# Performance work log

Measured on AMD Instinct MI355X. Metric: run time of the kernel, lower is better.

The kernel has to match this reference:

```python
import jax, jax.numpy as jnp
import numpy as np

B, T, F_, H1, H2, HEADS = 64, 128, 64, 32, 64, 4
E = H2 * F_  # embed_dim = hidden_dims[-1] * feats = 4096


def conv2d(x, w, b):
    # x: [b,c,H,W], w: [o,c,kh,kw], SAME padding (kernel 3 -> pad 1)
    y = jax.lax.conv_general_dilated(x, w, (1, 1), 'SAME',
                                     dimension_numbers=('NCHW', 'OIHW', 'NCHW'))
    return y + b[None, :, None, None]


def gru_layer(xs, h0, wg, bg, wc, bc):
    # xs: [b,t,c,H,W]; h0: [b,h,H,W]. Standard ConvGRU cell:
    #   r,u = sigmoid(conv([x,h])); cand = tanh(conv([x, r*h]))
    #   h' = (1-u)*h + u*cand
    def step(h, x):
        g = conv2d(jnp.concatenate([x, h], axis=1), wg, bg)
        r, u = jnp.split(jax.nn.sigmoid(g), 2, axis=1)
        cand = jnp.tanh(conv2d(jnp.concatenate([x, r * h], axis=1), wc, bc))
        h_next = (1.0 - u) * h + u * cand
        return h_next, h_next
    hT, ys = jax.lax.scan(step, h0, jnp.swapaxes(xs, 0, 1))
    return jnp.swapaxes(ys, 0, 1), hT  # [b,t,h,H,W], [b,h,H,W]


def mha(q, k, v, w_qkv, b_qkv, w_out, b_out):
    # q: [b,1,E], k/v: [b,t,E]; torch nn.MultiheadAttention (eval, no dropout)
    wq, wk, wv = jnp.split(w_qkv, 3, axis=0)
    bq, bk, bv = jnp.split(b_qkv, 3, axis=0)
    dh = E // HEADS
    def heads(x, w, bb):
        y = x @ w.T + bb
        b_, l_, _ = y.shape
        return y.reshape(b_, l_, HEADS, dh).transpose(0, 2, 1, 3)  # [b,h,l,dh]
    qh, kh, vh = heads(q, wq, bq), heads(k, wk, bk), heads(v, wv, bv)
    scores = jnp.einsum('bhqd,bhkd->bhqk', qh, kh) / jnp.sqrt(jnp.float32(dh))
    attn = jax.nn.softmax(scores, axis=-1)
    ctx = jnp.einsum('bhqk,bhkd->bhqd', attn, vh)
    ctx = ctx.transpose(0, 2, 1, 3).reshape(q.shape[0], q.shape[1], E)
    return ctx @ w_out.T + b_out


def setup_inputs() -> dict:
    key = jax.random.key(0)
    ks = jax.random.split(key, 24)
    s = 0.05
    d = {'x': jax.random.normal(ks[0], (B, T, F_), dtype=jnp.float32)}
    # encoder layer 0: in=1, h=H1; layer 1: in=H1, h=H2
    d['wg_e0'] = jax.random.normal(ks[1], (2 * H1, 1 + H1, 3, 3)) * s
    d['bg_e0'] = jnp.zeros((2 * H1,))
    d['wc_e0'] = jax.random.normal(ks[2], (H1, 1 + H1, 3, 3)) * s
    d['bc_e0'] = jnp.zeros((H1,))
    d['wg_e1'] = jax.random.normal(ks[3], (2 * H2, H1 + H2, 3, 3)) * s
    d['bg_e1'] = jnp.zeros((2 * H2,))
    d['wc_e1'] = jax.random.normal(ks[4], (H2, H1 + H2, 3, 3)) * s
    d['bc_e1'] = jnp.zeros((H2,))
    # decoder: input dim = 2*H2; hidden dims reversed [H2, H1]
    d['wg_d0'] = jax.random.normal(ks[5], (2 * H2, 2 * H2 + H2, 3, 3)) * s
    d['bg_d0'] = jnp.zeros((2 * H2,))
    d['wc_d0'] = jax.random.normal(ks[6], (H2, 2 * H2 + H2, 3, 3)) * s
    d['bc_d0'] = jnp.zeros((H2,))
    d['wg_d1'] = jax.random.normal(ks[7], (2 * H1, H2 + H1, 3, 3)) * s
    d['bg_d1'] = jnp.zeros((2 * H1,))
    d['wc_d1'] = jax.random.normal(ks[8], (H1, H2 + H1, 3, 3)) * s
    d['bc_d1'] = jnp.zeros((H1,))
    d['w_qkv'] = jax.random.normal(ks[9], (3 * E, E)) * (1.0 / np.sqrt(E))
    d['b_qkv'] = jnp.zeros((3 * E,))
    d['w_out'] = jax.random.normal(ks[10], (E, E)) * (1.0 / np.sqrt(E))
    d['b_out'] = jnp.zeros((E,))
    d['w_fin'] = jax.random.normal(ks[11], (1, H1, 1, 1)) * s
    d['b_fin'] = jnp.zeros((1,))
    return d


def reference(x, wg_e0, bg_e0, wc_e0, bc_e0, wg_e1, bg_e1, wc_e1, bc_e1,
              wg_d0, bg_d0, wc_d0, bc_d0, wg_d1, bg_d1, wc_d1, bc_d1,
              w_qkv, b_qkv, w_out, b_out, w_fin, b_fin):
    b, t, f = x.shape
    xr = x.reshape(b, t, 1, f, 1)
    # encoder (2 ConvGRU layers, zero init states)
    y0, h0 = gru_layer(xr, jnp.zeros((b, H1, f, 1), x.dtype), wg_e0, bg_e0, wc_e0, bc_e0)
    y1, h1 = gru_layer(y0, jnp.zeros((b, H2, f, 1), x.dtype), wg_e1, bg_e1, wc_e1, bc_e1)
    # attention bottleneck: query = last hidden, memory = encoder outputs
    query = h1.reshape(b, 1, E)
    memory = y1.reshape(b, t, E)
    context = mha(query, memory, memory, w_qkv, b_qkv, w_out, b_out)  # [b,1,E]
    ctx = context.reshape(b, 1, H2, f, 1)
    dec_in = jnp.concatenate([y1, jnp.broadcast_to(ctx, (b, t, H2, f, 1))], axis=2)
    # decoder init states: encoder last states reversed -> [h1 (H2), h0 (H1)]
    z0, _ = gru_layer(dec_in, h1, wg_d0, bg_d0, wc_d0, bc_d0)
    z1, _ = gru_layer(z0, h0, wg_d1, bg_d1, wc_d1, bc_d1)  # [b,t,H1,f,1]
    # final 1x1 conv applied per timestep == channel contraction
    rec = jnp.einsum('btcfw,oc->btofw', z1, w_fin[:, :, 0, 0]) + b_fin[None, None, :, None, None]
    return rec.reshape(b, t, f)
```

## Files before the change

kernel.cpp:

```cpp
#include <hip/hip_runtime.h>
#include <cstdint>


#define B_  64
#define T_  128
#define TC  32
#define NCH 4

__device__ __forceinline__ float wsum(float v) {
#pragma unroll
  for (int m = 32; m > 0; m >>= 1) v += __shfl_xor(v, m, 64);
  return v;
}
__device__ __forceinline__ float wmaxr(float v) {
#pragma unroll
  for (int m = 32; m > 0; m >>= 1) v = fmaxf(v, __shfl_xor(v, m, 64));
  return v;
}
__device__ __forceinline__ float sigmoidf_(float x) {
  return 1.f / (1.f + __expf(-x));
}
__device__ __forceinline__ float tanhf_(float x) {
  x = fminf(fmaxf(x, -15.f), 15.f);
  float e2 = __expf(2.f * x);
  return (e2 - 1.f) / (e2 + 1.f);
}

struct PackArgs {
  const float* src[16];
  float* dst[16];
  int intot[16];
  int ic0[16];
  int icn[16];
  int oc[16];
};

__global__ __launch_bounds__(256) void pack_all_kernel(PackArgs pa) {
  const int j = blockIdx.y;
  const int icN = pa.icn[j];
  const int total = pa.oc[j] * icN * 3;
  const int i = blockIdx.x * 256 + threadIdx.x;
  if (i >= total) return;
  const int per_oc = icN * 3;
  const int oc = i / per_oc;
  const int rem = i - oc * per_oc;
  const int ic = rem / 3, dk = rem - ic * 3;
  pa.dst[j][i] =
      pa.src[j][((size_t)(oc * pa.intot[j] + pa.ic0[j] + ic) * 3 + dk) * 3 + 1];
}

template <int INC, int OG, int OCC>
__device__ __forceinline__ void conv_x_body(
    float (*sin_)[72], int tid, int btl,
    const float* __restrict__ seq, int seqC, size_t sB,
    const float* __restrict__ ctx,
    const float* __restrict__ Wgx, const float* __restrict__ Wcx,
    const float* __restrict__ bg, const float* __restrict__ bc,
    float* __restrict__ out) {
  constexpr int OCT = OG + OCC;
  constexpr int NJ = OG / 32;
  constexpr int NJC = OCC / 32;
  const int b = btl >> 5;
  const int tl = btl & 31;
  const int ocg = tid >> 3;
  const int f0 = (tid & 7) << 3;

  for (int idx = tid; idx < INC * 72; idx += 256) {
    int ic = idx / 72, ff = idx - ic * 72;
    float v = 0.f;
    if (ff >= 1 && ff <= 64) {
      int fs = ff - 1;
      v = (ic < seqC)
              ? seq[(size_t)b * sB + (size_t)tl * seqC * 64 + ic * 64 + fs]
              : ctx[((size_t)b * (INC - seqC) + (ic - seqC)) * 64 + fs];
    }
    sin_[ic][ff] = v;
  }
  __syncthreads();

  if constexpr (INC >= 4) {
    {
      float acc[NJ][8];
#pragma unroll
      for (int j = 0; j < NJ; ++j) {
        float bb = bg[ocg + 32 * j];
#pragma unroll
        for (int ff = 0; ff < 8; ++ff) acc[j][ff] = bb;
      }
      for (int ic0 = 0; ic0 < INC; ic0 += 4) {
        float hv[4][10];
#pragma unroll
        for (int q = 0; q < 4; ++q) {
          float4 a4 = *(const float4*)&sin_[ic0 + q][f0];
          float4 b4 = *(const float4*)&sin_[ic0 + q][f0 + 4];
          float2 c2 = *(const float2*)&sin_[ic0 + q][f0 + 8];
          hv[q][0] = a4.x; hv[q][1] = a4.y; hv[q][2] = a4.z; hv[q][3] = a4.w;
          hv[q][4] = b4.x; hv[q][5] = b4.y; hv[q][6] = b4.z; hv[q][7] = b4.w;
          hv[q][8] = c2.x; hv[q][9] = c2.y;
        }
#pragma unroll
        for (int j = 0; j < NJ; ++j) {
          const int oc = ocg + 32 * j;
          const float4* w4 = (const float4*)(Wgx + ((size_t)oc * INC + ic0) * 3);
          float4 wa = w4[0], wb = w4[1], wc4 = w4[2];
          const float wt[12] = {wa.x, wa.y, wa.z, wa.w, wb.x, wb.y, wb.z, wb.w,
                                wc4.x, wc4.y, wc4.z, wc4.w};
#pragma unroll
          for (int q = 0; q < 4; ++q) {
            const float w0 = wt[3 * q], w1 = wt[3 * q + 1], w2 = wt[3 * q + 2];
#pragma unroll
            for (int ff = 0; ff < 8; ++ff)
              acc[j][ff] = fmaf(w0, hv[q][ff], fmaf(w1, hv[q][ff + 1], fmaf(w2, hv[q][ff + 2], acc[j][ff])));
          }
        }
      }
#pragma unroll
      for (int j = 0; j < NJ; ++j) {
        float* dst = out + ((size_t)btl * OCT + ocg + 32 * j) * 64 + f0;
        *(float4*)dst = make_float4(acc[j][0], acc[j][1], acc[j][2], acc[j][3]);
        *(float4*)(dst + 4) = make_float4(acc[j][4], acc[j][5], acc[j][6], acc[j][7]);
      }
    }
    {
      float acc[NJC][8];
#pragma unroll
      for (int j = 0; j < NJC; ++j) {
        float bb = bc[ocg + 32 * j];
#pragma unroll
        for (int ff = 0; ff < 8; ++ff) acc[j][ff] = bb;
      }
      for (int ic0 = 0; ic0 < INC; ic0 += 4) {
        float hv[4][10];
#pragma unroll
        for (int q = 0; q < 4; ++q) {
          float4 a4 = *(const float4*)&sin_[ic0 + q][f0];
          float4 b4 = *(const float4*)&sin_[ic0 + q][f0 + 4];
          float2 c2 = *(const float2*)&sin_[ic0 + q][f0 + 8];
          hv[q][0] = a4.x; hv[q][1] = a4.y; hv[q][2] = a4.z; hv[q][3] = a4.w;
          hv[q][4] = b4.x; hv[q][5] = b4.y; hv[q][6] = b4.z; hv[q][7] = b4.w;
          hv[q][8] = c2.x; hv[q][9] = c2.y;
        }
#pragma unroll
        for (int j = 0; j < NJC; ++j) {
          const int oc = ocg + 32 * j;
          const float4* w4 = (const float4*)(Wcx + ((size_t)oc * INC + ic0) * 3);
          float4 wa = w4[0], wb = w4[1], wc4 = w4[2];
          const float wt[12] = {wa.x, wa.y, wa.z, wa.w, wb.x, wb.y, wb.z, wb.w,
                                wc4.x, wc4.y, wc4.z, wc4.w};
#pragma unroll
          for (int q = 0; q < 4; ++q) {
            const float w0 = wt[3 * q], w1 = wt[3 * q + 1], w2 = wt[3 * q + 2];
#pragma unroll
            for (int ff = 0; ff < 8; ++ff)
              acc[j][ff] = fmaf(w0, hv[q][ff], fmaf(w1, hv[q][ff + 1], fmaf(w2, hv[q][ff + 2], acc[j][ff])));
          }
        }
      }
#pragma unroll
      for (int j = 0; j < NJC; ++j) {
        float* dst = out + ((size_t)btl * OCT + OG + ocg + 32 * j) * 64 + f0;
        *(float4*)dst = make_float4(acc[j][0], acc[j][1], acc[j][2], acc[j][3]);
        *(float4*)(dst + 4) = make_float4(acc[j][4], acc[j][5], acc[j][6], acc[j][7]);
      }
    }
  } else {
    float hv[10];
    {
      float4 a4 = *(const float4*)&sin_[0][f0];
      float4 b4 = *(const float4*)&sin_[0][f0 + 4];
      float2 c2 = *(const float2*)&sin_[0][f0 + 8];
      hv[0] = a4.x; hv[1] = a4.y; hv[2] = a4.z; hv[3] = a4.w;
      hv[4] = b4.x; hv[5] = b4.y; hv[6] = b4.z; hv[7] = b4.w;
      hv[8] = c2.x; hv[9] = c2.y;
    }
#pragma unroll
    for (int j = 0; j < NJ; ++j) {
      const int oc = ocg + 32 * j;
      const float w0 = Wgx[oc * 3], w1 = Wgx[oc * 3 + 1], w2 = Wgx[oc * 3 + 2];
      float acc[8];
#pragma unroll
      for (int ff = 0; ff < 8; ++ff)
        acc[ff] = fmaf(w0, hv[ff], fmaf(w1, hv[ff + 1], fmaf(w2, hv[ff + 2], bg[oc])));
      float* dst = out + ((size_t)btl * OCT + oc) * 64 + f0;
      *(float4*)dst = make_float4(acc[0], acc[1], acc[2], acc[3]);
      *(float4*)(dst + 4) = make_float4(acc[4], acc[5], acc[6], acc[7]);
    }
#pragma unroll
    for (int j = 0; j < NJC; ++j) {
      const int oc = ocg + 32 * j;
      const float w0 = Wcx[oc * 3], w1 = Wcx[oc * 3 + 1], w2 = Wcx[oc * 3 + 2];
      float acc[8];
#pragma unroll
      for (int ff = 0; ff < 8; ++ff)
        acc[ff] = fmaf(w0, hv[ff], fmaf(w1, hv[ff + 1], fmaf(w2, hv[ff + 2], bc[oc])));
      float* dst = out + ((size_t)btl * OCT + OG + oc) * 64 + f0;
      *(float4*)dst = make_float4(acc[0], acc[1], acc[2], acc[3]);
      *(float4*)(dst + 4) = make_float4(acc[4], acc[5], acc[6], acc[7]);
    }
  }
}

template <int INC, int OG, int OCC>
__global__ __launch_bounds__(256) void conv_x_kernel(
    const float* __restrict__ seq, int seqC, size_t sB,
    const float* __restrict__ ctx,
    const float* __restrict__ Wgx, const float* __restrict__ Wcx,
    const float* __restrict__ bg, const float* __restrict__ bc,
    float* __restrict__ out) {
  __shared__ float sin_[INC][72];
  conv_x_body<INC, OG, OCC>(sin_, threadIdx.x, blockIdx.x, seq, seqC, sB, ctx,
                            Wgx, Wcx, bg, bc, out);
}

__device__ __forceinline__ void final_body(
    int tid, int tile, const float* __restrict__ z1c,
    const float* __restrict__ wfin, const float* __restrict__ bfin,
    float* __restrict__ out, int tOff) {
  const int idx = tile * 256 + tid;
  const int f = idx & 63;
  const int tl = (idx >> 6) & 31;
  const int b = idx >> 11;
  const float* zp = z1c + ((size_t)b * TC + tl) * 2048 + f;
  float a = bfin[0];
#pragma unroll
  for (int c = 0; c < 32; ++c) a = fmaf(wfin[c], zp[c * 64], a);
  out[(size_t)b * 8192 + (size_t)(tOff + tl) * 64 + f] = a;
}

__global__ __launch_bounds__(256) void final_kernel(
    const float* __restrict__ z1c,
    const float* __restrict__ wfin, const float* __restrict__ bfin,
    float* __restrict__ out, int tOff) {
  final_body(threadIdx.x, blockIdx.x, z1c, wfin, bfin, out, tOff);
}

template <int HC>
__device__ __forceinline__ void gru_body(
    float* smem,
    const float* __restrict__ A, const float* __restrict__ Wgh,
    const float* __restrict__ Wch, const float* hinit,
    float* __restrict__ Y, size_t yB, float* hfinal, int b) {
  constexpr int NR = HC / 32;
  constexpr int OG = 2 * HC;
  constexpr int OCT = 3 * HC;
  float(*Hs)[68] = (float(*)[68])smem;
  float(*Rs)[68] = (float(*)[68])(smem + HC * 68);
  const int tid = threadIdx.x;
  const int ocg = tid >> 4;
  const int f0 = (tid & 15) << 2;
  const int im = (f0 == 0) ? 0 : f0 - 1;
  const bool lo = (f0 == 0), hi = (f0 == 60);

  float hreg[NR][4];
#pragma unroll
  for (int r = 0; r < NR; ++r) {
    const int oc = ocg + 32 * r;
    const float4 v = *(const float4*)(hinit + ((size_t)b * HC + oc) * 64 + f0);
    hreg[r][0] = v.x; hreg[r][1] = v.y; hreg[r][2] = v.z; hreg[r][3] = v.w;
    *(float4*)&Hs[oc][f0] = v;
  }
  __syncthreads();

  for (int tl = 0; tl < TC; ++tl) {
    const float* Abt = A + ((size_t)b * TC + tl) * (OCT * 64);
    float accr[NR][4], accu[NR][4], accc[NR][4];
#pragma unroll
    for (int r = 0; r < NR; ++r) {
      const int oc = ocg + 32 * r;
      const float4 vr = *(const float4*)(Abt + (size_t)oc * 64 + f0);
      const float4 vu = *(const float4*)(Abt + (size_t)(HC + oc) * 64 + f0);
      const float4 vc = *(const float4*)(Abt + (size_t)(OG + oc) * 64 + f0);
      accr[r][0] = vr.x; accr[r][1] = vr.y; accr[r][2] = vr.z; accr[r][3] = vr.w;
      accu[r][0] = vu.x; accu[r][1] = vu.y; accu[r][2] = vu.z; accu[r][3] = vu.w;
      accc[r][0] = vc.x; accc[r][1] = vc.y; accc[r][2] = vc.z; accc[r][3] = vc.w;
    }
#pragma unroll 2
    for (int hc0 = 0; hc0 < HC; hc0 += 4) {
      float hv[4][6];
#pragma unroll
      for (int q = 0; q < 4; ++q) {
        const float4 h4 = *(const float4*)&Hs[hc0 + q][f0];
        const float lf = Hs[hc0 + q][im];
        const float rt = Hs[hc0 + q][f0 + 4];
        hv[q][0] = lo ? 0.f : lf;
        hv[q][1] = h4.x; hv[q][2] = h4.y; hv[q][3] = h4.z; hv[q][4] = h4.w;
        hv[q][5] = hi ? 0.f : rt;
      }
#pragma unroll
      for (int r = 0; r < NR; ++r) {
        {
          const float4* w4 = (const float4*)(Wgh + ((size_t)(ocg + 32 * r) * HC + hc0) * 3);
          const float4 wa = w4[0], wb = w4[1], wc4 = w4[2];
          const float wt[12] = {wa.x, wa.y, wa.z, wa.w, wb.x, wb.y, wb.z, wb.w,
                                wc4.x, wc4.y, wc4.z, wc4.w};
#pragma unroll
          for (int q = 0; q < 4; ++q) {
            const float w0 = wt[3 * q], w1 = wt[3 * q + 1], w2 = wt[3 * q + 2];
#pragma unroll
            for (int ff = 0; ff < 4; ++ff)
              accr[r][ff] = fmaf(w0, hv[q][ff], fmaf(w1, hv[q][ff + 1], fmaf(w2, hv[q][ff + 2], accr[r][ff])));
          }
        }
        {
          const float4* w4 = (const float4*)(Wgh + ((size_t)(HC + ocg + 32 * r) * HC + hc0) * 3);
          const float4 wa = w4[0], wb = w4[1], wc4 = w4[2];
          const float wt[12] = {wa.x, wa.y, wa.z, wa.w, wb.x, wb.y, wb.z, wb.w,
                                wc4.x, wc4.y, wc4.z, wc4.w};
#pragma unroll
          for (int q = 0; q < 4; ++q) {
            const float w0 = wt[3 * q], w1 = wt[3 * q + 1], w2 = wt[3 * q + 2];
#pragma unroll
            for (int ff = 0; ff < 4; ++ff)
              accu[r][ff] = fmaf(w0, hv[q][ff], fmaf(w1, hv[q][ff + 1], fmaf(w2, hv[q][ff + 2], accu[r][ff])));
          }
        }
      }
    }
    float uu[NR][4];
#pragma unroll
    for (int r = 0; r < NR; ++r) {
      float4 rh;
#pragma unroll
      for (int ff = 0; ff < 4; ++ff) {
        uu[r][ff] = sigmoidf_(accu[r][ff]);
        (&rh.x)[ff] = sigmoidf_(accr[r][ff]) * hreg[r][ff];
      }
      *(float4*)&Rs[ocg + 32 * r][f0] = rh;
    }
    __syncthreads();
#pragma unroll 2
    for (int hc0 = 0; hc0 < HC; hc0 += 4) {
      float hv[4][6];
#pragma unroll
      for (int q = 0; q < 4; ++q) {
        const float4 h4 = *(const float4*)&Rs[hc0 + q][f0];
        const float lf = Rs[hc0 + q][im];
        const float rt = Rs[hc0 + q][f0 + 4];
        hv[q][0] = lo ? 0.f : lf;
        hv[q][1] = h4.x; hv[q][2] = h4.y; hv[q][3] = h4.z; hv[q][4] = h4.w;
        hv[q][5] = hi ? 0.f : rt;
      }
#pragma unroll
      for (int r = 0; r < NR; ++r) {
        const float4* w4 = (const float4*)(Wch + ((size_t)(ocg + 32 * r) * HC + hc0) * 3);
        const float4 wa = w4[0], wb = w4[1], wc4 = w4[2];
        const float wt[12] = {wa.x, wa.y, wa.z, wa.w, wb.x, wb.y, wb.z, wb.w,
                              wc4.x, wc4.y, wc4.z, wc4.w};
#pragma unroll
        for (int q = 0; q < 4; ++q) {
          const float w0 = wt[3 * q], w1 = wt[3 * q + 1], w2 = wt[3 * q + 2];
#pragma unroll
          for (int ff = 0; ff < 4; ++ff)
            accc[r][ff] = fmaf(w0, hv[q][ff], fmaf(w1, hv[q][ff + 1], fmaf(w2, hv[q][ff + 2], accc[r][ff])));
        }
      }
    }
#pragma unroll
    for (int r = 0; r < NR; ++r) {
      const int oc = ocg + 32 * r;
      float4 yv;
#pragma unroll
      for (int ff = 0; ff < 4; ++ff) {
        const float cd = tanhf_(accc[r][ff]);
        const float hn = fmaf(uu[r][ff], cd - hreg[r][ff], hreg[r][ff]);
        hreg[r][ff] = hn;
        (&yv.x)[ff] = hn;
      }
      *(float4*)(Y + (size_t)b * yB + (size_t)tl * (HC * 64) + (size_t)oc * 64 + f0) = yv;
      *(float4*)&Hs[oc][f0] = yv;
    }
    __syncthreads();
  }
#pragma unroll
  for (int r = 0; r < NR; ++r) {
    const int oc = ocg + 32 * r;
    *(float4*)(hfinal + ((size_t)b * HC + oc) * 64 + f0) =
        make_float4(hreg[r][0], hreg[r][1], hreg[r][2], hreg[r][3]);
  }
}

template <int HC>
__global__ __launch_bounds__(512) void gru_rec_kernel(
    const float* __restrict__ A, const float* __restrict__ Wgh,
    const float* __restrict__ Wch, const float* hinit,
    float* __restrict__ Y, size_t yB, float* hfinal) {
  __shared__ float smem[2 * HC * 68];
  gru_body<HC>(smem, A, Wgh, Wch, hinit, Y, yB, hfinal, blockIdx.x);
}

struct GruArgs {
  const float* A;
  const float* Wgh;
  const float* Wch;
  const float* hinit;
  float* Y;
  size_t yB;
  float* hfinal;
};

__global__ __launch_bounds__(512) void gru_fused_kernel(GruArgs g64, GruArgs g32) {
  __shared__ float smem[2 * 64 * 68];
  if (blockIdx.x < 64) {
    gru_body<64>(smem, g64.A, g64.Wgh, g64.Wch, g64.hinit, g64.Y, g64.yB,
                 g64.hfinal, blockIdx.x);
  } else {
    gru_body<32>(smem, g32.A, g32.Wgh, g32.Wch, g32.hinit, g32.Y, g32.yB,
                 g32.hfinal, blockIdx.x - 64);
  }
}

struct ConvJob {
  int kind;
  int nblk;
  const float* seq;
  int seqC;
  size_t sB;
  const float* ctx;
  const float* w0;
  const float* w1;
  const float* b0;
  const float* b1;
  float* out;
  int tOff;
};

struct MegaArgs {
  GruArgs g64;
  GruArgs g32;
  int ng64, ng32, njobs;
  ConvJob jobs[4];
};

__global__ __launch_bounds__(512) void mega_kernel(MegaArgs ma) {
  __shared__ float smem[18432];
  int bid = blockIdx.x;
  if (bid < ma.ng64) {
    gru_body<64>(smem, ma.g64.A, ma.g64.Wgh, ma.g64.Wch, ma.g64.hinit,
                 ma.g64.Y, ma.g64.yB, ma.g64.hfinal, bid);
    return;
  }
  bid -= ma.ng64;
  if (bid < ma.ng32) {
    gru_body<32>(smem, ma.g32.A, ma.g32.Wgh, ma.g32.Wch, ma.g32.hinit,
                 ma.g32.Y, ma.g32.yB, ma.g32.hfinal, bid);
    return;
  }
  bid -= ma.ng32;
  const int half = threadIdx.x >> 8;
  const int tid = threadIdx.x & 255;
#pragma unroll 1
  for (int j = 0; j < ma.njobs; ++j) {
    if (bid < ma.jobs[j].nblk) {
      const ConvJob cj = ma.jobs[j];
      const int tile = bid * 2 + half;
      if (cj.kind == 2) {
        conv_x_body<128, 128, 64>((float(*)[72])(smem + half * 128 * 72), tid,
                                  tile, cj.seq, cj.seqC, cj.sB, cj.ctx, cj.w0,
                                  cj.w1, cj.b0, cj.b1, cj.out);
      } else if (cj.kind == 3) {
        conv_x_body<64, 64, 32>((float(*)[72])(smem + half * 64 * 72), tid,
                                tile, cj.seq, cj.seqC, cj.sB, cj.ctx, cj.w0,
                                cj.w1, cj.b0, cj.b1, cj.out);
      } else {
        final_body(tid, tile, cj.seq, cj.w0, cj.b0, cj.out, cj.tOff);
      }
      return;
    }
    bid -= ma.jobs[j].nblk;
  }
}

template <bool WT>
__global__ __launch_bounds__(256) void gemm64_kernel(
    const float* __restrict__ W, int wrs,
    const float* __restrict__ X, int xrs,
    float* __restrict__ O, int ors,
    const float* __restrict__ bias, int K,
    int ebh, size_t hsW, size_t hsX, size_t hsO, size_t hsB) {
  int eb = blockIdx.x;
  if (ebh > 0) {
    int h = blockIdx.x / ebh;
    eb = blockIdx.x - h * ebh;
    W += h * hsW; X += h * hsX; O += h * hsO;
    if (bias) bias += h * hsB;
  }
  const int e0 = eb * 64;
  __shared__ float Xs[64][68];
  __shared__ float Ws[64][68];
  const int tb4 = (threadIdx.x & 15) << 2;
  const int te4 = (threadIdx.x >> 4) << 2;
  float acc[4][4] = {};
  for (int k0 = 0; k0 < K; k0 += 64) {
    {
      const int row = threadIdx.x >> 2;
      const int kq = (threadIdx.x & 3) << 4;
      const float* src = X + (size_t)row * xrs + k0 + kq;
#pragma unroll
      for (int q = 0; q < 4; ++q) {
        float4 v = *(const float4*)(src + (q << 2));
        Xs[kq + (q << 2) + 0][row] = v.x;
        Xs[kq + (q << 2) + 1][row] = v.y;
        Xs[kq + (q << 2) + 2][row] = v.z;
        Xs[kq + (q << 2) + 3][row] = v.w;
      }
    }
    if (!WT) {
      const int row = threadIdx.x >> 2;
      const int kq = (threadIdx.x & 3) << 4;
      const float* src = W + (size_t)(e0 + row) * wrs + k0 + kq;
#pragma unroll
      for (int q = 0; q < 4; ++q) {
        float4 v = *(const float4*)(src + (q << 2));
        Ws[kq + (q << 2) + 0][row] = v.x;
        Ws[kq + (q << 2) + 1][row] = v.y;
        Ws[kq + (q << 2) + 2][row] = v.z;
        Ws[kq + (q << 2) + 3][row] = v.w;
      }
    } else {
      const int row = threadIdx.x >> 2;
      const int eq = (threadIdx.x & 3) << 4;
      const float* src = W + (size_t)(k0 + row) * wrs + e0 + eq;
#pragma unroll
      for (int q = 0; q < 4; ++q)
        *(float4*)&Ws[row][eq + (q << 2)] = *(const float4*)(src + (q << 2));
    }
    __syncthreads();
#pragma unroll 8
    for (int k = 0; k < 64; ++k) {
      float4 xv = *(const float4*)&Xs[k][tb4];
      float4 wv4 = *(const float4*)&Ws[k][te4];
      const float xb[4] = {xv.x, xv.y, xv.z, xv.w};
      const float we[4] = {wv4.x, wv4.y, wv4.z, wv4.w};
#pragma unroll
      for (int i = 0; i < 4; ++i)
#pragma unroll
        for (int j = 0; j < 4; ++j) acc[i][j] = fmaf(xb[i], we[j], acc[i][j]);
    }
    __syncthreads();
  }
#pragma unroll
  for (int i = 0; i < 4; ++i)
#pragma unroll
    for (int j = 0; j < 4; ++j) {
      float v = acc[i][j];
      if (bias) v += bias[e0 + te4 + j];
      O[(size_t)(tb4 + i) * ors + e0 + te4 + j] = v;
    }
}

__global__ __launch_bounds__(256) void attn_scores_kernel(
    const float* __restrict__ qkh, const float* __restrict__ mem,
    float* __restrict__ scores) {
  const int b = blockIdx.x >> 4;
  const int tt = blockIdx.x & 15;
  const int h = threadIdx.x >> 6;
  const int lane = threadIdx.x & 63;
  const float4* qk4 = (const float4*)(qkh + ((size_t)b * 4 + h) * 4096);
#pragma unroll 2
  for (int ti = 0; ti < 8; ++ti) {
    const int t = tt * 8 + ti;
    const float4* m4 = (const float4*)(mem + ((size_t)b * 128 + t) * 4096);
    float s = 0.f;
    for (int e = lane; e < 1024; e += 64) {
      float4 q = qk4[e], m = m4[e];
      s = fmaf(q.x, m.x, fmaf(q.y, m.y, fmaf(q.z, m.z, fmaf(q.w, m.w, s))));
    }
    s = wsum(s);
    if (lane == 0) scores[((size_t)b * 4 + h) * 128 + t] = s;
  }
}

__global__ __launch_bounds__(256) void attn_softmax_kernel(
    const float* __restrict__ scores, const float* __restrict__ qbuf,
    const float* __restrict__ bqkv, float* __restrict__ attnp) {
  const int b = blockIdx.x;
  const int h = threadIdx.x >> 6;
  const int lane = threadIdx.x & 63;
  const float4* q4 = (const float4*)(qbuf + (size_t)b * 4096 + h * 1024);
  const float4* k4 = (const float4*)(bqkv + 4096 + h * 1024);
  float qb = 0.f;
#pragma unroll
  for (int d = lane; d < 256; d += 64) {
    float4 q = q4[d], k = k4[d];
    qb = fmaf(q.x, k.x, fmaf(q.y, k.y, fmaf(q.z, k.z, fmaf(q.w, k.w, qb))));
  }
  qb = wsum(qb);
  const float* sc = scores + ((size_t)b * 4 + h) * 128;
  float s0 = (sc[lane] + qb) * 0.03125f;
  float s1 = (sc[lane + 64] + qb) * 0.03125f;
  float mx = wmaxr(fmaxf(s0, s1));
  float e0v = __expf(s0 - mx), e1v = __expf(s1 - mx);
  float inv = 1.f / wsum(e0v + e1v);
  attnp[((size_t)b * 4 + h) * 128 + lane] = e0v * inv;
  attnp[((size_t)b * 4 + h) * 128 + lane + 64] = e1v * inv;
}

__global__ __launch_bounds__(256) void attn_wsum_kernel(
    const float* __restrict__ attnp, const float* __restrict__ mem,
    float* __restrict__ wmem) {
  const int b = blockIdx.x >> 4;
  const int eb = blockIdx.x & 15;
  const int e = eb * 256 + threadIdx.x;
  __shared__ float ap[4][128];
  for (int i = threadIdx.x; i < 512; i += 256)
    ap[i >> 7][i & 127] = attnp[(size_t)b * 512 + i];
  __syncthreads();
  float a0 = 0, a1 = 0, a2 = 0, a3 = 0;
  const float* mb = mem + (size_t)b * 128 * 4096 + e;
#pragma unroll 4
  for (int t = 0; t < 128; ++t) {
    float m = mb[(size_t)t * 4096];
    a0 = fmaf(ap[0][t], m, a0);
    a1 = fmaf(ap[1][t], m, a1);
    a2 = fmaf(ap[2][t], m, a2);
    a3 = fmaf(ap[3][t], m, a3);
  }
  wmem[((size_t)b * 4 + 0) * 4096 + e] = a0;
  wmem[((size_t)b * 4 + 1) * 4096 + e] = a1;
  wmem[((size_t)b * 4 + 2) * 4096 + e] = a2;
  wmem[((size_t)b * 4 + 3) * 4096 + e] = a3;
}

extern "C" void kernel_launch(void* const* d_in, const int* in_sizes, int n_in,
                              void* d_out, int out_size, void* d_ws, size_t ws_size,
                              hipStream_t stream) {
  (void)in_sizes; (void)n_in; (void)out_size;
  const float* x     = (const float*)d_in[0];
  const float* wg_e0 = (const float*)d_in[1];
  const float* bg_e0 = (const float*)d_in[2];
  const float* wc_e0 = (const float*)d_in[3];
  const float* bc_e0 = (const float*)d_in[4];
  const float* wg_e1 = (const float*)d_in[5];
  const float* bg_e1 = (const float*)d_in[6];
  const float* wc_e1 = (const float*)d_in[7];
  const float* bc_e1 = (const float*)d_in[8];
  const float* wg_d0 = (const float*)d_in[9];
  const float* bg_d0 = (const float*)d_in[10];
  const float* wc_d0 = (const float*)d_in[11];
  const float* bc_d0 = (const float*)d_in[12];
  const float* wg_d1 = (const float*)d_in[13];
  const float* bg_d1 = (const float*)d_in[14];
  const float* wc_d1 = (const float*)d_in[15];
  const float* bc_d1 = (const float*)d_in[16];
  const float* w_qkv = (const float*)d_in[17];
  const float* b_qkv = (const float*)d_in[18];
  const float* w_out = (const float*)d_in[19];
  const float* b_out = (const float*)d_in[20];
  const float* w_fin = (const float*)d_in[21];
  const float* b_fin = (const float*)d_in[22];
  float* out = (float*)d_out;

  float* WS = (float*)d_ws;
  size_t off = 0;
  auto alloc = [&](size_t n) { float* p = WS + off; off += (n + 63) & ~(size_t)63; return p; };
  float* Amp0 = alloc((size_t)B_ * TC * 192 * 64);
  float* A960 = alloc((size_t)B_ * TC * 96 * 64);
  float* Y0c  = alloc((size_t)B_ * TC * 32 * 64);
  float* Y1   = alloc((size_t)B_ * T_ * 64 * 64);
  float* Z0p[2] = {alloc((size_t)B_ * TC * 64 * 64), alloc((size_t)B_ * TC * 64 * 64)};
  float* Z1p0 = alloc((size_t)B_ * TC * 32 * 64);
  float* He0p[2] = {alloc((size_t)B_ * 32 * 64), alloc((size_t)B_ * 32 * 64)};
  float* He1p[2] = {alloc((size_t)B_ * 64 * 64), alloc((size_t)B_ * 64 * 64)};
  float* Hd0p[2] = {alloc((size_t)B_ * 64 * 64), alloc((size_t)B_ * 64 * 64)};
  float* Hd1p[2] = {alloc((size_t)B_ * 32 * 64), alloc((size_t)B_ * 32 * 64)};
  float* QBUF = alloc((size_t)B_ * 4096);
  float* QKH  = alloc((size_t)B_ * 4 * 4096);
  float* WMEM = alloc((size_t)B_ * 4 * 4096);
  float* CTXB = alloc((size_t)B_ * 4096);
  float* CTXO = alloc((size_t)B_ * 4096);
  float* SCR  = alloc((size_t)B_ * 4 * 128);
  float* ATTN = alloc((size_t)B_ * 4 * 128);
  float* wgx_e0 = alloc(64 * 1 * 3);    float* wgh_e0 = alloc(64 * 32 * 3);
  float* wcx_e0 = alloc(32 * 1 * 3);    float* wch_e0 = alloc(32 * 32 * 3);
  float* wgx_e1 = alloc(128 * 32 * 3);  float* wgh_e1 = alloc(128 * 64 * 3);
  float* wcx_e1 = alloc(64 * 32 * 3);   float* wch_e1 = alloc(64 * 64 * 3);
  float* wgx_d0 = alloc(128 * 128 * 3); float* wgh_d0 = alloc(128 * 64 * 3);
  float* wcx_d0 = alloc(64 * 128 * 3);  float* wch_d0 = alloc(64 * 64 * 3);
  float* wgx_d1 = alloc(64 * 64 * 3);   float* wgh_d1 = alloc(64 * 32 * 3);
  float* wcx_d1 = alloc(32 * 64 * 3);   float* wch_d1 = alloc(32 * 32 * 3);
  const size_t off_r9 = off;
  float* Amp1 = alloc((size_t)B_ * TC * 192 * 64);
  float* A961 = alloc((size_t)B_ * TC * 96 * 64);
  float* Z1p1 = alloc((size_t)B_ * TC * 32 * 64);
  const size_t off_full = off;
  if (ws_size < off_r9 * sizeof(float)) return;
  const bool mega_ok = (ws_size >= off_full * sizeof(float));

  float* Amp[2] = {Amp0, Amp1};
  float* A96p[2] = {A960, A961};
  float* Z1p[2] = {Z1p0, Z1p1};

  {
    PackArgs pa;
    const float* srcs[16] = {wg_e0, wg_e0, wc_e0, wc_e0, wg_e1, wg_e1, wc_e1, wc_e1,
                             wg_d0, wg_d0, wc_d0, wc_d0, wg_d1, wg_d1, wc_d1, wc_d1};
    float* dsts[16] = {wgx_e0, wgh_e0, wcx_e0, wch_e0, wgx_e1, wgh_e1, wcx_e1, wch_e1,
                       wgx_d0, wgh_d0, wcx_d0, wch_d0, wgx_d1, wgh_d1, wcx_d1, wch_d1};
    int intot[16] = {33, 33, 33, 33, 96, 96, 96, 96, 192, 192, 192, 192, 96, 96, 96, 96};
    int ic0[16]   = {0, 1, 0, 1, 0, 32, 0, 32, 0, 128, 0, 128, 0, 64, 0, 64};
    int icn[16]   = {1, 32, 1, 32, 32, 64, 32, 64, 128, 64, 128, 64, 64, 32, 64, 32};
    int occ[16]   = {64, 64, 32, 32, 128, 128, 64, 64, 128, 128, 64, 64, 64, 64, 32, 32};
    for (int j = 0; j < 16; ++j) {
      pa.src[j] = srcs[j]; pa.dst[j] = dsts[j];
      pa.intot[j] = intot[j]; pa.ic0[j] = ic0[j]; pa.icn[j] = icn[j]; pa.oc[j] = occ[j];
    }
    pack_all_kernel<<<dim3(192, 16), 256, 0, stream>>>(pa);
  }

  hipMemsetAsync(He0p[0], 0, (size_t)B_ * 32 * 64 * 4, stream);
  hipMemsetAsync(He1p[0], 0, (size_t)B_ * 64 * 64 * 4, stream);

  auto conv_e0 = [&](int c) {
    conv_x_kernel<1, 64, 32><<<2048, 256, 0, stream>>>(
        x + (size_t)c * TC * 64, 1, (size_t)T_ * 64, nullptr,
        wgx_e0, wcx_e0, bg_e0, bc_e0, A96p[0]);
  };
  auto conv_e1 = [&]() {
    conv_x_kernel<32, 128, 64><<<2048, 256, 0, stream>>>(
        Y0c, 32, (size_t)TC * 32 * 64, nullptr,
        wgx_e1, wcx_e1, bg_e1, bc_e1, Amp[0]);
  };

  conv_e0(0);
  gru_rec_kernel<32><<<64, 512, 0, stream>>>(
      A96p[0], wgh_e0, wch_e0, He0p[0], Y0c, (size_t)TC * 2048, He0p[1]);
  conv_e1();
  for (int c = 0; c < NCH; ++c) {
    GruArgs g64 = {Amp[0], wgh_e1, wch_e1, He1p[c & 1],
                   Y1 + (size_t)c * TC * 4096, (size_t)T_ * 4096, He1p[(c + 1) & 1]};
    if (c < NCH - 1) {
      conv_e0(c + 1);
      GruArgs g32 = {A96p[0], wgh_e0, wch_e0, He0p[(c + 1) & 1],
                     Y0c, (size_t)TC * 2048, He0p[c & 1]};
      gru_fused_kernel<<<128, 512, 0, stream>>>(g64, g32);
      conv_e1();
    } else {
      gru_rec_kernel<64><<<64, 512, 0, stream>>>(
          g64.A, g64.Wgh, g64.Wch, g64.hinit, g64.Y, g64.yB, g64.hfinal);
    }
  }
  float* He0f = He0p[0];
  float* He1f = He1p[0];

  const float* wq = w_qkv;
  const float* wk = w_qkv + (size_t)4096 * 4096;
  const float* wv = w_qkv + (size_t)8192 * 4096;
  gemm64_kernel<false><<<64, 256, 0, stream>>>(wq, 4096, He1f, 4096, QBUF, 4096,
                                               b_qkv, 4096, 0, 0, 0, 0, 0);
  gemm64_kernel<true><<<256, 256, 0, stream>>>(wk, 4096, QBUF, 4096, QKH, 16384,
                                               nullptr, 1024, 64,
                                               (size_t)1024 * 4096, 1024, 4096, 0);
  attn_scores_kernel<<<B_ * 16, 256, 0, stream>>>(QKH, Y1, SCR);
  attn_softmax_kernel<<<B_, 256, 0, stream>>>(SCR, QBUF, b_qkv, ATTN);
  attn_wsum_kernel<<<B_ * 16, 256, 0, stream>>>(ATTN, Y1, WMEM);
  gemm64_kernel<false><<<64, 256, 0, stream>>>(wv, 4096, WMEM, 16384, CTXB, 4096,
                                               b_qkv + 8192, 4096, 16,
                                               (size_t)1024 * 4096, 4096, 1024, 1024);
  gemm64_kernel<false><<<64, 256, 0, stream>>>(w_out, 4096, CTXB, 4096, CTXO, 4096,
                                               b_out, 4096, 0, 0, 0, 0, 0);

  if (mega_ok) {
    auto JD0 = [&](int c, float* dst) {
      ConvJob j{}; j.kind = 2; j.nblk = 1024;
      j.seq = Y1 + (size_t)c * TC * 4096; j.seqC = 64; j.sB = (size_t)T_ * 4096;
      j.ctx = CTXO; j.w0 = wgx_d0; j.w1 = wcx_d0; j.b0 = bg_d0; j.b1 = bc_d0;
      j.out = dst; return j;
    };
    auto JD1 = [&](float* z0src, float* dst) {
      ConvJob j{}; j.kind = 3; j.nblk = 1024;
      j.seq = z0src; j.seqC = 64; j.sB = (size_t)TC * 4096;
      j.ctx = nullptr; j.w0 = wgx_d1; j.w1 = wcx_d1; j.b0 = bg_d1; j.b1 = bc_d1;
      j.out = dst; return j;
    };
    auto JFIN = [&](float* z1src, int tOff) {
      ConvJob j{}; j.kind = 4; j.nblk = 256;
      j.seq = z1src; j.w0 = w_fin; j.b0 = b_fin; j.out = out; j.tOff = tOff;
      return j;
    };
    auto mega = [&](const GruArgs* a64, const GruArgs* a32, int nj,
                    const ConvJob* js) {
      MegaArgs ma{};
      ma.ng64 = a64 ? 64 : 0; if (a64) ma.g64 = *a64;
      ma.ng32 = a32 ? 64 : 0; if (a32) ma.g32 = *a32;
      ma.njobs = nj;
      int grid = ma.ng64 + ma.ng32;
      for (int i = 0; i < nj; ++i) { ma.jobs[i] = js[i]; grid += js[i].nblk; }
      mega_kernel<<<grid, 512, 0, stream>>>(ma);
    };

    GruArgs gd0[4], gd1[4];
    for (int c = 0; c < 4; ++c) {
      gd0[c] = {Amp[c & 1], wgh_d0, wch_d0,
                (c == 0 ? He1f : Hd0p[c & 1]),
                Z0p[c & 1], (size_t)TC * 4096, Hd0p[(c + 1) & 1]};
      gd1[c] = {A96p[c & 1], wgh_d1, wch_d1,
                (c == 0 ? He0f : Hd1p[c & 1]),
                Z1p[c & 1], (size_t)TC * 2048, Hd1p[(c + 1) & 1]};
    }

    conv_x_kernel<128, 128, 64><<<2048, 256, 0, stream>>>(
        Y1, 64, (size_t)T_ * 4096, CTXO, wgx_d0, wcx_d0, bg_d0, bc_d0, Amp[0]);
    { ConvJob js[1] = {JD0(1, Amp[1])};
      mega(&gd0[0], nullptr, 1, js); }
    { ConvJob js[2] = {JD1(Z0p[0], A96p[0]), JD0(2, Amp[0])};
      mega(&gd0[1], nullptr, 2, js); }
    { ConvJob js[2] = {JD1(Z0p[1], A96p[1]), JD0(3, Amp[1])};
      mega(&gd0[2], &gd1[0], 2, js); }
    { ConvJob js[2] = {JD1(Z0p[0], A96p[0]), JFIN(Z1p[0], 0)};
      mega(&gd0[3], &gd1[1], 2, js); }
    { ConvJob js[2] = {JD1(Z0p[1], A96p[1]), JFIN(Z1p[1], TC)};
      mega(nullptr, &gd1[2], 2, js); }
    { ConvJob js[1] = {JFIN(Z1p[0], 2 * TC)};
      mega(nullptr, &gd1[3], 1, js); }
    final_kernel<<<512, 256, 0, stream>>>(Z1p[1], w_fin, b_fin, out, 3 * TC);
  } else {
    auto conv_d0 = [&](int c) {
      conv_x_kernel<128, 128, 64><<<2048, 256, 0, stream>>>(
          Y1 + (size_t)c * TC * 4096, 64, (size_t)T_ * 4096, CTXO,
          wgx_d0, wcx_d0, bg_d0, bc_d0, Amp[0]);
    };
    auto conv_d1 = [&](int c) {
      conv_x_kernel<64, 64, 32><<<2048, 256, 0, stream>>>(
          Z0p[c & 1], 64, (size_t)TC * 4096, nullptr,
          wgx_d1, wcx_d1, bg_d1, bc_d1, A96p[0]);
    };
    conv_d0(0);
    gru_rec_kernel<64><<<64, 512, 0, stream>>>(
        Amp[0], wgh_d0, wch_d0, He1f, Z0p[0], (size_t)TC * 4096, Hd0p[1]);
    conv_d1(0);
    for (int c = 1; c < NCH; ++c) {
      conv_d0(c);
      GruArgs g64 = {Amp[0], wgh_d0, wch_d0, Hd0p[c & 1],
                     Z0p[c & 1], (size_t)TC * 4096, Hd0p[(c + 1) & 1]};
      GruArgs g32 = {A96p[0], wgh_d1, wch_d1,
                     (c - 1 == 0 ? He0f : Hd1p[(c - 1) & 1]),
                     Z1p[0], (size_t)TC * 2048, Hd1p[c & 1]};
      gru_fused_kernel<<<128, 512, 0, stream>>>(g64, g32);
      final_kernel<<<512, 256, 0, stream>>>(Z1p[0], w_fin, b_fin, out, (c - 1) * TC);
      conv_d1(c);
    }
    gru_rec_kernel<32><<<64, 512, 0, stream>>>(
        A96p[0], wgh_d1, wch_d1, Hd1p[1], Z1p[0], (size_t)TC * 2048, Hd1p[0]);
    final_kernel<<<512, 256, 0, stream>>>(Z1p[0], w_fin, b_fin, out, 3 * TC);
  }
}
```

Measured before the change: 7.721 ms.

## Pipeline encoder GRU chunks with conv jobs in mega kernel launches

Moves the encoder phase onto the same mega-kernel scheduling already used by the decoder. Layer-0 and layer-1 input convolutions now run as jobs inside the same launches as the recurrent GRU blocks, and a double-buffered Y0 buffer lets layer-0 and layer-1 recurrences of different chunks run concurrently. This is meant to hide the serial recurrence latency behind the parallel conv work and to cut the number of launches, at the cost of extra workspace and more block types sharing one grid.

```diff
diff --git a/kernel.cpp b/kernel.cpp
--- a/kernel.cpp
+++ b/kernel.cpp
@@ -453,7 +453,15 @@
     if (bid < ma.jobs[j].nblk) {
       const ConvJob cj = ma.jobs[j];
       const int tile = bid * 2 + half;
-      if (cj.kind == 2) {
+      if (cj.kind == 0) {
+        conv_x_body<1, 64, 32>((float(*)[72])(smem + half * 1 * 72), tid,
+                               tile, cj.seq, cj.seqC, cj.sB, cj.ctx, cj.w0,
+                               cj.w1, cj.b0, cj.b1, cj.out);
+      } else if (cj.kind == 1) {
+        conv_x_body<32, 128, 64>((float(*)[72])(smem + half * 32 * 72), tid,
+                                 tile, cj.seq, cj.seqC, cj.sB, cj.ctx, cj.w0,
+                                 cj.w1, cj.b0, cj.b1, cj.out);
+      } else if (cj.kind == 2) {
         conv_x_body<128, 128, 64>((float(*)[72])(smem + half * 128 * 72), tid,
                                   tile, cj.seq, cj.seqC, cj.sB, cj.ctx, cj.w0,
                                   cj.w1, cj.b0, cj.b1, cj.out);
@@ -655,7 +663,7 @@
   auto alloc = [&](size_t n) { float* p = WS + off; off += (n + 63) & ~(size_t)63; return p; };
   float* Amp0 = alloc((size_t)B_ * TC * 192 * 64);
   float* A960 = alloc((size_t)B_ * TC * 96 * 64);
-  float* Y0c  = alloc((size_t)B_ * TC * 32 * 64);
+  float* Y0p0 = alloc((size_t)B_ * TC * 32 * 64);
   float* Y1   = alloc((size_t)B_ * T_ * 64 * 64);
   float* Z0p[2] = {alloc((size_t)B_ * TC * 64 * 64), alloc((size_t)B_ * TC * 64 * 64)};
   float* Z1p0 = alloc((size_t)B_ * TC * 32 * 64);
@@ -682,6 +690,7 @@
   float* Amp1 = alloc((size_t)B_ * TC * 192 * 64);
   float* A961 = alloc((size_t)B_ * TC * 96 * 64);
   float* Z1p1 = alloc((size_t)B_ * TC * 32 * 64);
+  float* Y0p1 = alloc((size_t)B_ * TC * 32 * 64);
   const size_t off_full = off;
   if (ws_size < off_r9 * sizeof(float)) return;
   const bool mega_ok = (ws_size >= off_full * sizeof(float));
@@ -689,6 +698,7 @@
   float* Amp[2] = {Amp0, Amp1};
   float* A96p[2] = {A960, A961};
   float* Z1p[2] = {Z1p0, Z1p1};
+  float* Y0p[2] = {Y0p0, Y0p1};
 
   {
     PackArgs pa;
@@ -710,33 +720,97 @@
   hipMemsetAsync(He0p[0], 0, (size_t)B_ * 32 * 64 * 4, stream);
   hipMemsetAsync(He1p[0], 0, (size_t)B_ * 64 * 64 * 4, stream);
 
-  auto conv_e0 = [&](int c) {
-    conv_x_kernel<1, 64, 32><<<2048, 256, 0, stream>>>(
-        x + (size_t)c * TC * 64, 1, (size_t)T_ * 64, nullptr,
-        wgx_e0, wcx_e0, bg_e0, bc_e0, A96p[0]);
+  auto mega = [&](const GruArgs* a64, const GruArgs* a32, int nj,
+                  const ConvJob* js) {
+    MegaArgs ma{};
+    ma.ng64 = a64 ? 64 : 0; if (a64) ma.g64 = *a64;
+    ma.ng32 = a32 ? 64 : 0; if (a32) ma.g32 = *a32;
+    ma.njobs = nj;
+    int grid = ma.ng64 + ma.ng32;
+    for (int i = 0; i < nj; ++i) { ma.jobs[i] = js[i]; grid += js[i].nblk; }
+    mega_kernel<<<grid, 512, 0, stream>>>(ma);
   };
-  auto conv_e1 = [&]() {
-    conv_x_kernel<32, 128, 64><<<2048, 256, 0, stream>>>(
-        Y0c, 32, (size_t)TC * 32 * 64, nullptr,
-        wgx_e1, wcx_e1, bg_e1, bc_e1, Amp[0]);
+  auto JE0 = [&](int c, float* dst) {
+    ConvJob j{}; j.kind = 0; j.nblk = 1024;
+    j.seq = x + (size_t)c * TC * 64; j.seqC = 1; j.sB = (size_t)T_ * 64;
+    j.ctx = nullptr; j.w0 = wgx_e0; j.w1 = wcx_e0; j.b0 = bg_e0; j.b1 = bc_e0;
+    j.out = dst; return j;
   };
-
-  conv_e0(0);
-  gru_rec_kernel<32><<<64, 512, 0, stream>>>(
-      A96p[0], wgh_e0, wch_e0, He0p[0], Y0c, (size_t)TC * 2048, He0p[1]);
-  conv_e1();
-  for (int c = 0; c < NCH; ++c) {
-    GruArgs g64 = {Amp[0], wgh_e1, wch_e1, He1p[c & 1],
-                   Y1 + (size_t)c * TC * 4096, (size_t)T_ * 4096, He1p[(c + 1) & 1]};
-    if (c < NCH - 1) {
-      conv_e0(c + 1);
-      GruArgs g32 = {A96p[0], wgh_e0, wch_e0, He0p[(c + 1) & 1],
-                     Y0c, (size_t)TC * 2048, He0p[c & 1]};
-      gru_fused_kernel<<<128, 512, 0, stream>>>(g64, g32);
-      conv_e1();
-    } else {
-      gru_rec_kernel<64><<<64, 512, 0, stream>>>(
-          g64.A, g64.Wgh, g64.Wch, g64.hinit, g64.Y, g64.yB, g64.hfinal);
+  auto JE1 = [&](float* y0src, float* dst) {
+    ConvJob j{}; j.kind = 1; j.nblk = 1024;
+    j.seq = y0src; j.seqC = 32; j.sB = (size_t)TC * 2048;
+    j.ctx = nullptr; j.w0 = wgx_e1; j.w1 = wcx_e1; j.b0 = bg_e1; j.b1 = bc_e1;
+    j.out = dst; return j;
+  };
+  auto JD0 = [&](int c, float* dst) {
+    ConvJob j{}; j.kind = 2; j.nblk = 1024;
+    j.seq = Y1 + (size_t)c * TC * 4096; j.seqC = 64; j.sB = (size_t)T_ * 4096;
+    j.ctx = CTXO; j.w0 = wgx_d0; j.w1 = wcx_d0; j.b0 = bg_d0; j.b1 = bc_d0;
+    j.out = dst; return j;
+  };
+  auto JD1 = [&](float* z0src, float* dst) {
+    ConvJob j{}; j.kind = 3; j.nblk = 1024;
+    j.seq = z0src; j.seqC = 64; j.sB = (size_t)TC * 4096;
+    j.ctx = nullptr; j.w0 = wgx_d1; j.w1 = wcx_d1; j.b0 = bg_d1; j.b1 = bc_d1;
+    j.out = dst; return j;
+  };
+  auto JFIN = [&](float* z1src, int tOff) {
+    ConvJob j{}; j.kind = 4; j.nblk = 256;
+    j.seq = z1src; j.w0 = w_fin; j.b0 = b_fin; j.out = out; j.tOff = tOff;
+    return j;
+  };
+
+  if (mega_ok) {
+    GruArgs ge32[4], ge64[4];
+    for (int c = 0; c < 4; ++c) {
+      ge32[c] = {A96p[c & 1], wgh_e0, wch_e0, He0p[c & 1],
+                 Y0p[c & 1], (size_t)TC * 2048, He0p[(c + 1) & 1]};
+      ge64[c] = {Amp[c & 1], wgh_e1, wch_e1, He1p[c & 1],
+                 Y1 + (size_t)c * TC * 4096, (size_t)T_ * 4096, He1p[(c + 1) & 1]};
+    }
+    { ConvJob js[2] = {JE0(0, A96p[0]), JE0(1, A96p[1])};
+      mega(nullptr, nullptr, 2, js); }
+    gru_rec_kernel<32><<<64, 512, 0, stream>>>(
+        A96p[0], wgh_e0, wch_e0, He0p[0], Y0p[0], (size_t)TC * 2048, He0p[1]);
+    { ConvJob js[2] = {JE1(Y0p[0], Amp[0]), JE0(2, A96p[0])};
+      mega(nullptr, &ge32[1], 2, js); }
+    { ConvJob js[2] = {JE1(Y0p[1], Amp[1]), JE0(3, A96p[1])};
+      mega(&ge64[0], &ge32[2], 2, js); }
+    { ConvJob js[1] = {JE1(Y0p[0], Amp[0])};
+      mega(&ge64[1], &ge32[3], 1, js); }
+    { ConvJob js[1] = {JE1(Y0p[1], Amp[1])};
+      mega(&ge64[2], nullptr, 1, js); }
+    gru_rec_kernel<64><<<64, 512, 0, stream>>>(
+        Amp[1], wgh_e1, wch_e1, He1p[1], Y1 + (size_t)3 * TC * 4096,
+        (size_t)T_ * 4096, He1p[0]);
+  } else {
+    auto conv_e0 = [&](int c) {
+      conv_x_kernel<1, 64, 32><<<2048, 256, 0, stream>>>(
+          x + (size_t)c * TC * 64, 1, (size_t)T_ * 64, nullptr,
+          wgx_e0, wcx_e0, bg_e0, bc_e0, A96p[0]);
+    };
+    auto conv_e1 = [&]() {
+      conv_x_kernel<32, 128, 64><<<2048, 256, 0, stream>>>(
+          Y0p[0], 32, (size_t)TC * 2048, nullptr,
+          wgx_e1, wcx_e1, bg_e1, bc_e1, Amp[0]);
+    };
+    conv_e0(0);
+    gru_rec_kernel<32><<<64, 512, 0, stream>>>(
+        A96p[0], wgh_e0, wch_e0, He0p[0], Y0p[0], (size_t)TC * 2048, He0p[1]);
+    conv_e1();
+    for (int c = 0; c < NCH; ++c) {
+      GruArgs g64 = {Amp[0], wgh_e1, wch_e1, He1p[c & 1],
+                     Y1 + (size_t)c * TC * 4096, (size_t)T_ * 4096, He1p[(c + 1) & 1]};
+      if (c < NCH - 1) {
+        conv_e0(c + 1);
+        GruArgs g32 = {A96p[0], wgh_e0, wch_e0, He0p[(c + 1) & 1],
+                       Y0p[0], (size_t)TC * 2048, He0p[c & 1]};
+        gru_fused_kernel<<<128, 512, 0, stream>>>(g64, g32);
+        conv_e1();
+      } else {
+        gru_rec_kernel<64><<<64, 512, 0, stream>>>(
+            g64.A, g64.Wgh, g64.Wch, g64.hinit, g64.Y, g64.yB, g64.hfinal);
+      }
     }
   }
   float* He0f = He0p[0];
@@ -760,34 +834,6 @@
                                                b_out, 4096, 0, 0, 0, 0, 0);
 
   if (mega_ok) {
-    auto JD0 = [&](int c, float* dst) {
-      ConvJob j{}; j.kind = 2; j.nblk = 1024;
-      j.seq = Y1 + (size_t)c * TC * 4096; j.seqC = 64; j.sB = (size_t)T_ * 4096;
-      j.ctx = CTXO; j.w0 = wgx_d0; j.w1 = wcx_d0; j.b0 = bg_d0; j.b1 = bc_d0;
-      j.out = dst; return j;
-    };
-    auto JD1 = [&](float* z0src, float* dst) {
-      ConvJob j{}; j.kind = 3; j.nblk = 1024;
-      j.seq = z0src; j.seqC = 64; j.sB = (size_t)TC * 4096;
-      j.ctx = nullptr; j.w0 = wgx_d1; j.w1 = wcx_d1; j.b0 = bg_d1; j.b1 = bc_d1;
-      j.out = dst; return j;
-    };
-    auto JFIN = [&](float* z1src, int tOff) {
-      ConvJob j{}; j.kind = 4; j.nblk = 256;
-      j.seq = z1src; j.w0 = w_fin; j.b0 = b_fin; j.out = out; j.tOff = tOff;
-      return j;
-    };
-    auto mega = [&](const GruArgs* a64, const GruArgs* a32, int nj,
-                    const ConvJob* js) {
-      MegaArgs ma{};
-      ma.ng64 = a64 ? 64 : 0; if (a64) ma.g64 = *a64;
-      ma.ng32 = a32 ? 64 : 0; if (a32) ma.g32 = *a32;
-      ma.njobs = nj;
-      int grid = ma.ng64 + ma.ng32;
-      for (int i = 0; i < nj; ++i) { ma.jobs[i] = js[i]; grid += js[i].nblk; }
-      mega_kernel<<<grid, 512, 0, stream>>>(ma);
-    };
-
     GruArgs gd0[4], gd1[4];
     for (int c = 0; c < 4; ++c) {
       gd0[c] = {Amp[c & 1], wgh_d0, wch_d0,
@@ -797,7 +843,6 @@
                 (c == 0 ? He0f : Hd1p[c & 1]),
                 Z1p[c & 1], (size_t)TC * 2048, Hd1p[(c + 1) & 1]};
     }
-
     conv_x_kernel<128, 128, 64><<<2048, 256, 0, stream>>>(
         Y1, 64, (size_t)T_ * 4096, CTXO, wgx_d0, wcx_d0, bg_d0, bc_d0, Amp[0]);
     { ConvJob js[1] = {JD0(1, Amp[1])};
```

Measured after the change: 7.740 ms. About the same (+0.2%).
